# Kernel tuning notes

Hardware: AMD Instinct MI355X
Metric: run time of the kernel (lower is better)

The kernel has to match this reference:

```python
import jax, jax.numpy as jnp
import numpy as np

MASK_VAL = -2.0**32 + 1


def setup_inputs() -> dict:
    key = jax.random.key(0)
    ks = jax.random.split(key, 5)
    b, h, L, d = 4, 8, 256, 64
    return {
        "Q": jax.random.normal(ks[0], (b, h, L, d), dtype=jnp.float32),
        "K": jax.random.normal(ks[1], (b, h, L, d), dtype=jnp.float32),
        "V": jax.random.normal(ks[2], (b, h, L, d), dtype=jnp.float32),
        "time_matrix_K": jax.random.normal(ks[3], (b, h, L, L, d), dtype=jnp.float32),
        "time_matrix_V": jax.random.normal(ks[4], (b, h, L, L, d), dtype=jnp.float32),
        "attn_mask": jnp.zeros((L, L), dtype=jnp.float32),
        "padding_mask": jnp.zeros((b, L), dtype=bool),
    }


def reference(Q, K, V, time_matrix_K, time_matrix_V, attn_mask, padding_mask):
    scale = jnp.sqrt(jnp.asarray(Q.shape[-1], Q.dtype))
    # content score + relative-time key score
    energy = jnp.einsum("bhqd,bhkd->bhqk", Q, K)
    energy = energy + jnp.einsum("bhqkd,bhqd->bhqk", time_matrix_K, Q)
    energy = energy / scale
    if attn_mask is not None:
        energy = energy + attn_mask[None, None, :, :]
    if padding_mask is not None:
        energy = jnp.where(padding_mask[:, None, None, :], jnp.asarray(MASK_VAL, energy.dtype), energy)
    attention_weight = jax.nn.softmax(energy, axis=-1)
    # value aggregation + relative-time value aggregation
    O = jnp.einsum("bhqk,bhkd->bhqd", attention_weight, V)
    O = O + jnp.einsum("bhqk,bhqkd->bhqd", attention_weight, time_matrix_V)
    return O, attention_weight
```

## Files before the change

### kernel.cpp

```cpp
#include <hip/hip_runtime.h>

#define L_SEQ 256
#define D_HEAD 64
#define MASK_VAL (-4294967295.0f)

__global__ __launch_bounds__(256) void ta_sdp_kernel(
    const float* __restrict__ Q, const float* __restrict__ K,
    const float* __restrict__ V, const float* __restrict__ tmK,
    const float* __restrict__ tmV, const float* __restrict__ amask,
    const unsigned char* __restrict__ pmask,
    float* __restrict__ O_out, float* __restrict__ W_out)
{
    const int row = blockIdx.x;
    const int q   = row & (L_SEQ - 1);
    const int bh  = row >> 8;
    const int b   = bh >> 3;

    const int t   = threadIdx.x;
    const int dd4 = t & 15;
    const int kg  = t >> 4;

    const float4* Q4  = (const float4*)(Q   + (size_t)row * D_HEAD);
    const float4* K4  = (const float4*)(K   + (size_t)bh * L_SEQ * D_HEAD);
    const float4* V4  = (const float4*)(V   + (size_t)bh * L_SEQ * D_HEAD);
    const float4* tK4 = (const float4*)(tmK + (size_t)row * L_SEQ * D_HEAD);
    const float4* tV4 = (const float4*)(tmV + (size_t)row * L_SEQ * D_HEAD);

    __shared__ float  s_e[L_SEQ];
    __shared__ float  s_red[8];
    __shared__ float4 s_acc[256];

    const float4 q4 = Q4[dd4];

#pragma unroll 4
    for (int k0 = 0; k0 < 16; ++k0) {
        const int k  = k0 * 16 + kg;
        const int i4 = k * (D_HEAD / 4) + dd4;
        const float4 a = tK4[i4];
        const float4 c = K4[i4];
        float p = (a.x + c.x) * q4.x + (a.y + c.y) * q4.y
                + (a.z + c.z) * q4.z + (a.w + c.w) * q4.w;
        p += __shfl_xor(p, 1);
        p += __shfl_xor(p, 2);
        p += __shfl_xor(p, 4);
        p += __shfl_xor(p, 8);
        if (dd4 == 0) s_e[k] = p;
    }
    __syncthreads();

    float e = s_e[t] * 0.125f + amask[q * L_SEQ + t];
    if (pmask[b * L_SEQ + t]) e = MASK_VAL;

    float m = e;
#pragma unroll
    for (int off = 32; off; off >>= 1) m = fmaxf(m, __shfl_xor(m, off));
    if ((t & 63) == 0) s_red[t >> 6] = m;
    __syncthreads();
    m = fmaxf(fmaxf(s_red[0], s_red[1]), fmaxf(s_red[2], s_red[3]));

    const float p = __expf(e - m);
    float s = p;
#pragma unroll
    for (int off = 32; off; off >>= 1) s += __shfl_xor(s, off);
    if ((t & 63) == 0) s_red[4 + (t >> 6)] = s;
    __syncthreads();
    s = (s_red[4] + s_red[5]) + (s_red[6] + s_red[7]);

    const float w = p / s;
    W_out[(size_t)row * L_SEQ + t] = w;
    s_e[t] = w;
    __syncthreads();

    float4 acc = make_float4(0.f, 0.f, 0.f, 0.f);
#pragma unroll 4
    for (int k0 = 0; k0 < 16; ++k0) {
        const int k  = k0 * 16 + kg;
        const float wk = s_e[k];
        const int i4 = k * (D_HEAD / 4) + dd4;
        const float4 a = tV4[i4];
        const float4 c = V4[i4];
        acc.x += wk * (a.x + c.x);
        acc.y += wk * (a.y + c.y);
        acc.z += wk * (a.z + c.z);
        acc.w += wk * (a.w + c.w);
    }
    s_acc[t] = acc;
    __syncthreads();

#pragma unroll
    for (int s2 = 8; s2 > 0; s2 >>= 1) {
        if (kg < s2) {
            const float4 o = s_acc[t + s2 * 16];
            acc.x += o.x; acc.y += o.y; acc.z += o.z; acc.w += o.w;
            s_acc[t] = acc;
        }
        __syncthreads();
    }
    if (kg == 0) {
        ((float4*)(O_out + (size_t)row * D_HEAD))[dd4] = acc;
    }
}

extern "C" void kernel_launch(void* const* d_in, const int* in_sizes, int n_in,
                              void* d_out, int out_size, void* d_ws, size_t ws_size,
                              hipStream_t stream) {
    const float*         Q     = (const float*)d_in[0];
    const float*         K     = (const float*)d_in[1];
    const float*         V     = (const float*)d_in[2];
    const float*         tmK   = (const float*)d_in[3];
    const float*         tmV   = (const float*)d_in[4];
    const float*         amask = (const float*)d_in[5];
    const unsigned char* pmask = (const unsigned char*)d_in[6];

    float* O_out = (float*)d_out;
    float* W_out = (float*)d_out + in_sizes[0];

    const int rows = 4 * 8 * L_SEQ;
    ta_sdp_kernel<<<dim3(rows), dim3(256), 0, stream>>>(
        Q, K, V, tmK, tmV, amask, pmask, O_out, W_out);
}
```

Measured before the change: 996.4 us.

## Split fused attention into energy/softmax and output kernels

Splits the single kernel into two launches: one computes energies and the softmax weights, the other streams tmV/V using the stored weights to produce O. The aim is to let each kernel keep more loads in flight without the mid-kernel softmax barriers stalling the tmV stream. It also swaps the per-row shuffle reduction for a padded shared-memory partial-sum array, raises unroll to 8, and replaces the 4-step tree reduction with two 4-way steps. The cost is a second launch and a round trip of the weights through global memory.

```diff
diff --git a/kernel.cpp b/kernel.cpp
--- a/kernel.cpp
+++ b/kernel.cpp
@@ -4,12 +4,10 @@
 #define D_HEAD 64
 #define MASK_VAL (-4294967295.0f)
 
-__global__ __launch_bounds__(256) void ta_sdp_kernel(
+__global__ __launch_bounds__(256) void ta_energy_softmax(
     const float* __restrict__ Q, const float* __restrict__ K,
-    const float* __restrict__ V, const float* __restrict__ tmK,
-    const float* __restrict__ tmV, const float* __restrict__ amask,
-    const unsigned char* __restrict__ pmask,
-    float* __restrict__ O_out, float* __restrict__ W_out)
+    const float* __restrict__ tmK, const float* __restrict__ amask,
+    const unsigned char* __restrict__ pmask, float* __restrict__ W_out)
 {
     const int row = blockIdx.x;
     const int q   = row & (L_SEQ - 1);
@@ -20,19 +18,16 @@
     const int dd4 = t & 15;
     const int kg  = t >> 4;
 
+    __shared__ float s_part[L_SEQ][17];
+    __shared__ float s_red[8];
+
     const float4* Q4  = (const float4*)(Q   + (size_t)row * D_HEAD);
     const float4* K4  = (const float4*)(K   + (size_t)bh * L_SEQ * D_HEAD);
-    const float4* V4  = (const float4*)(V   + (size_t)bh * L_SEQ * D_HEAD);
     const float4* tK4 = (const float4*)(tmK + (size_t)row * L_SEQ * D_HEAD);
-    const float4* tV4 = (const float4*)(tmV + (size_t)row * L_SEQ * D_HEAD);
-
-    __shared__ float  s_e[L_SEQ];
-    __shared__ float  s_red[8];
-    __shared__ float4 s_acc[256];
 
     const float4 q4 = Q4[dd4];
 
-#pragma unroll 4
+#pragma unroll 8
     for (int k0 = 0; k0 < 16; ++k0) {
         const int k  = k0 * 16 + kg;
         const int i4 = k * (D_HEAD / 4) + dd4;
@@ -40,15 +35,14 @@
         const float4 c = K4[i4];
         float p = (a.x + c.x) * q4.x + (a.y + c.y) * q4.y
                 + (a.z + c.z) * q4.z + (a.w + c.w) * q4.w;
-        p += __shfl_xor(p, 1);
-        p += __shfl_xor(p, 2);
-        p += __shfl_xor(p, 4);
-        p += __shfl_xor(p, 8);
-        if (dd4 == 0) s_e[k] = p;
+        s_part[k][dd4] = p;
     }
     __syncthreads();
 
-    float e = s_e[t] * 0.125f + amask[q * L_SEQ + t];
+    float e = 0.f;
+#pragma unroll
+    for (int j = 0; j < 16; ++j) e += s_part[t][j];
+    e = e * 0.125f + amask[q * L_SEQ + t];
     if (pmask[b * L_SEQ + t]) e = MASK_VAL;
 
     float m = e;
@@ -66,19 +60,40 @@
     __syncthreads();
     s = (s_red[4] + s_red[5]) + (s_red[6] + s_red[7]);
 
-    const float w = p / s;
-    W_out[(size_t)row * L_SEQ + t] = w;
-    s_e[t] = w;
+    W_out[(size_t)row * L_SEQ + t] = p / s;
+}
+
+__global__ __launch_bounds__(256) void ta_output(
+    const float* __restrict__ V, const float* __restrict__ tmV,
+    const float* __restrict__ W, float* __restrict__ O_out)
+{
+    const int row = blockIdx.x;
+    const int bh  = row >> 8;
+    const int t   = threadIdx.x;
+    const int dd4 = t & 15;
+    const int kg  = t >> 4;
+
+    __shared__ float  s_w[L_SEQ];
+    __shared__ float4 s_acc[256];
+
+    s_w[t] = W[(size_t)row * L_SEQ + t];
     __syncthreads();
 
+    float wreg[16];
+#pragma unroll
+    for (int k0 = 0; k0 < 16; ++k0) wreg[k0] = s_w[k0 * 16 + kg];
+
+    const float4* V4  = (const float4*)(V   + (size_t)bh * L_SEQ * D_HEAD);
+    const float4* tV4 = (const float4*)(tmV + (size_t)row * L_SEQ * D_HEAD);
+
     float4 acc = make_float4(0.f, 0.f, 0.f, 0.f);
-#pragma unroll 4
+#pragma unroll 8
     for (int k0 = 0; k0 < 16; ++k0) {
         const int k  = k0 * 16 + kg;
-        const float wk = s_e[k];
         const int i4 = k * (D_HEAD / 4) + dd4;
         const float4 a = tV4[i4];
         const float4 c = V4[i4];
+        const float wk = wreg[k0];
         acc.x += wk * (a.x + c.x);
         acc.y += wk * (a.y + c.y);
         acc.z += wk * (a.z + c.z);
@@ -87,17 +102,28 @@
     s_acc[t] = acc;
     __syncthreads();
 
-#pragma unroll
-    for (int s2 = 8; s2 > 0; s2 >>= 1) {
-        if (kg < s2) {
-            const float4 o = s_acc[t + s2 * 16];
-            acc.x += o.x; acc.y += o.y; acc.z += o.z; acc.w += o.w;
-            s_acc[t] = acc;
-        }
-        __syncthreads();
+    if (t < 64) {
+        float4 r = s_acc[t];
+        const float4 r1 = s_acc[t + 64];
+        const float4 r2 = s_acc[t + 128];
+        const float4 r3 = s_acc[t + 192];
+        r.x += r1.x + r2.x + r3.x;
+        r.y += r1.y + r2.y + r3.y;
+        r.z += r1.z + r2.z + r3.z;
+        r.w += r1.w + r2.w + r3.w;
+        s_acc[t] = r;
     }
-    if (kg == 0) {
-        ((float4*)(O_out + (size_t)row * D_HEAD))[dd4] = acc;
+    __syncthreads();
+    if (t < 16) {
+        float4 r = s_acc[t];
+        const float4 r1 = s_acc[t + 16];
+        const float4 r2 = s_acc[t + 32];
+        const float4 r3 = s_acc[t + 48];
+        r.x += r1.x + r2.x + r3.x;
+        r.y += r1.y + r2.y + r3.y;
+        r.z += r1.z + r2.z + r3.z;
+        r.w += r1.w + r2.w + r3.w;
+        ((float4*)(O_out + (size_t)row * D_HEAD))[t] = r;
     }
 }
 
@@ -116,6 +142,8 @@
     float* W_out = (float*)d_out + in_sizes[0];
 
     const int rows = 4 * 8 * L_SEQ;
-    ta_sdp_kernel<<<dim3(rows), dim3(256), 0, stream>>>(
-        Q, K, V, tmK, tmV, amask, pmask, O_out, W_out);
+    ta_energy_softmax<<<dim3(rows), dim3(256), 0, stream>>>(
+        Q, K, tmK, amask, pmask, W_out);
+    ta_output<<<dim3(rows), dim3(256), 0, stream>>>(
+        V, tmV, W_out, O_out);
 }
```

Result: no change. 987.0 us (-0.9%).
